# Optimization experiments

Measured on AMD Instinct MI355X. Metric: run time of the kernel, lower is better.

Reference implementation:

```python
import jax, jax.numpy as jnp
import numpy as np

N_NODES = 80000
N_EDGES = 1280000
NODE_DIM = 32
EDGE_DIM = 16
HIDDEN = 64
N_HIDDEN_LAYERS = 3  # layer_count - 1
NUM_GRAPHS = 256


def setup_inputs() -> dict:
    key = jax.random.key(0)
    ks = jax.random.split(key, 16)
    s = 0.05
    H = jax.random.normal(ks[0], (N_NODES, NODE_DIM), dtype=jnp.float32)
    Xe = jax.random.normal(ks[1], (N_EDGES, EDGE_DIM), dtype=jnp.float32)
    id_Xe = jax.random.randint(ks[2], (2, N_EDGES), 0, N_NODES, dtype=jnp.int32).astype(jnp.int64)
    batch_idx = jnp.sort(jax.random.randint(ks[3], (N_NODES,), 0, NUM_GRAPHS, dtype=jnp.int32)).astype(jnp.int64)
    # input layer: M: (node+edge)->hidden, U: (hidden+node)->hidden
    Mw0 = jax.random.normal(ks[4], (NODE_DIM + EDGE_DIM, HIDDEN), dtype=jnp.float32) * s
    Mb0 = jnp.zeros((HIDDEN,), dtype=jnp.float32)
    Uw0 = jax.random.normal(ks[5], (HIDDEN + NODE_DIM, HIDDEN), dtype=jnp.float32) * s
    Ub0 = jnp.zeros((HIDDEN,), dtype=jnp.float32)
    # hidden layers: M: (hidden+edge)->hidden, U: (2*hidden)->hidden (stacked)
    Mw_h = jax.random.normal(ks[6], (N_HIDDEN_LAYERS, HIDDEN + EDGE_DIM, HIDDEN), dtype=jnp.float32) * s
    Mb_h = jnp.zeros((N_HIDDEN_LAYERS, HIDDEN), dtype=jnp.float32)
    Uw_h = jax.random.normal(ks[7], (N_HIDDEN_LAYERS, 2 * HIDDEN, HIDDEN), dtype=jnp.float32) * s
    Ub_h = jnp.zeros((N_HIDDEN_LAYERS, HIDDEN), dtype=jnp.float32)
    # final linear head hidden -> 1
    Ww = jax.random.normal(ks[8], (HIDDEN, 1), dtype=jnp.float32) * s
    Wb = jnp.zeros((1,), dtype=jnp.float32)
    return {"H": H, "Xe": Xe, "id_Xe": id_Xe, "batch_idx": batch_idx,
            "Mw0": Mw0, "Mb0": Mb0, "Uw0": Uw0, "Ub0": Ub0,
            "Mw_h": Mw_h, "Mb_h": Mb_h, "Uw_h": Uw_h, "Ub_h": Ub_h,
            "Ww": Ww, "Wb": Wb}


def reference(H, Xe, id_Xe, batch_idx, Mw0, Mb0, Uw0, Ub0, Mw_h, Mb_h, Uw_h, Ub_h, Ww, Wb):
    n = H.shape[0]
    src = id_Xe[0]
    dst = id_Xe[1]

    def gnn_layer(h, Mw, Mb, Uw, Ub):
        # message: gather source node features, concat edge features, MLP M
        m = jax.nn.relu(jnp.concatenate([h[src], Xe], axis=-1) @ Mw + Mb)  # [E, hidden]
        # scatter-sum to target nodes
        agg = jax.ops.segment_sum(m, dst, num_segments=n)  # [N, hidden]
        # update: concat node state with aggregated message, MLP U
        return jax.nn.relu(jnp.concatenate([h, agg], axis=-1) @ Uw + Ub)

    y = gnn_layer(H, Mw0, Mb0, Uw0, Ub0)
    for i in range(Mw_h.shape[0]):
        y = gnn_layer(y, Mw_h[i], Mb_h[i], Uw_h[i], Ub_h[i])

    pooled = jax.ops.segment_sum(y, batch_idx, num_segments=NUM_GRAPHS)  # [G, hidden]
    return pooled @ Ww + Wb  # [G, 1]
```

## Files before the change

kernel.cpp:

```cpp
#include <hip/hip_runtime.h>
#include <hip/hip_fp16.h>

#define HID 64

struct alignas(8)  H4 { __half2 a, b; };
struct alignas(16) H8 { __half2 h[4]; };

typedef _Float16 h2n __attribute__((ext_vector_type(2)));

__device__ inline float dot2f(__half2 a, __half2 b, float c) {
#if __has_builtin(__builtin_amdgcn_fdot2)
    h2n an, bn;
    __builtin_memcpy(&an, &a, 4);
    __builtin_memcpy(&bn, &b, 4);
    return __builtin_amdgcn_fdot2(an, bn, c, false);
#else
    float2 af = __half22float2(a), bf = __half22float2(b);
    return c + af.x * bf.x + af.y * bf.y;
#endif
}

__global__ __launch_bounds__(256) void deg_count(const int* __restrict__ dst,
                                                 int* __restrict__ deg, int E) {
    int e = blockIdx.x * 256 + threadIdx.x;
    if (e < E) atomicAdd(&deg[dst[e]], 1);
}

__global__ __launch_bounds__(256) void scan1(const int* __restrict__ deg,
                                             int* __restrict__ rowptr,
                                             int* __restrict__ bsums, int N) {
    __shared__ int s[256];
    const int t = threadIdx.x;
    const int base = blockIdx.x * 2048 + t * 8;
    int v[8], tot = 0;
    #pragma unroll
    for (int i = 0; i < 8; i++) {
        int x = (base + i < N) ? deg[base + i] : 0;
        v[i] = tot; tot += x;
    }
    s[t] = tot; __syncthreads();
    for (int off = 1; off < 256; off <<= 1) {
        int a = (t >= off) ? s[t - off] : 0;
        __syncthreads(); s[t] += a; __syncthreads();
    }
    const int texcl = s[t] - tot;
    #pragma unroll
    for (int i = 0; i < 8; i++)
        if (base + i < N) rowptr[base + i] = texcl + v[i];
    if (t == 255) bsums[blockIdx.x] = s[255];
}

__global__ void scan2(int* bsums, int NB) {
    if (blockIdx.x == 0 && threadIdx.x == 0) {
        int run = 0;
        for (int i = 0; i < NB; i++) { int x = bsums[i]; bsums[i] = run; run += x; }
    }
}

__global__ __launch_bounds__(256) void scan3(int* __restrict__ rowptr,
                                             const int* __restrict__ bsums,
                                             int N, int E) {
    int idx = blockIdx.x * 256 + threadIdx.x;
    if (idx < N) rowptr[idx] += bsums[idx >> 11];
    if (idx == 0) rowptr[N] = E;
}

__global__ __launch_bounds__(256) void permute_k(
    const int* __restrict__ src, const int* __restrict__ dst,
    const int* __restrict__ rowptr, int* __restrict__ cursor,
    const float* __restrict__ Xe, __half* __restrict__ Xes,
    unsigned* __restrict__ pks, int E)
{
    int e = blockIdx.x * 256 + threadIdx.x;
    if (e >= E) return;
    int d = dst[e];
    int pos = rowptr[d] + atomicAdd(&cursor[d], 1);
    pks[pos] = ((unsigned)src[e] << 5) | (unsigned)(d & 31);
    const float4* xi = (const float4*)&Xe[(size_t)e * 16];
    float4 x0 = xi[0], x1 = xi[1], x2 = xi[2], x3 = xi[3];
    H8 h0, h1;
    h0.h[0] = __float22half2_rn(make_float2(x0.x, x0.y));
    h0.h[1] = __float22half2_rn(make_float2(x0.z, x0.w));
    h0.h[2] = __float22half2_rn(make_float2(x1.x, x1.y));
    h0.h[3] = __float22half2_rn(make_float2(x1.z, x1.w));
    h1.h[0] = __float22half2_rn(make_float2(x2.x, x2.y));
    h1.h[1] = __float22half2_rn(make_float2(x2.z, x2.w));
    h1.h[2] = __float22half2_rn(make_float2(x3.x, x3.y));
    h1.h[3] = __float22half2_rn(make_float2(x3.z, x3.w));
    H8* xo = (H8*)&Xes[(size_t)pos * 16];
    xo[0] = h0; xo[1] = h1;
}

template<int K1>
__global__ __launch_bounds__(256) void pm_dual(
    const float* __restrict__ Hn,
    const float* __restrict__ Wm, const float* __restrict__ bm,
    const float* __restrict__ Wu, const float* __restrict__ bu,
    __half* __restrict__ PMh, __half* __restrict__ Th, int N)
{
    constexpr int KP = K1 + 4;
    constexpr int P4 = K1 / 4;
    __shared__ float Ws[K1 * 128];
    __shared__ float Xs[32 * KP];

    const int tid = threadIdx.x;
    for (int i = tid; i < K1 * 32; i += 256) {
        const int row = i >> 5, c4 = i & 31;
        float4 v = (c4 < 16) ? *(const float4*)&Wm[row * 64 + c4 * 4]
                             : *(const float4*)&Wu[row * 64 + (c4 - 16) * 4];
        *(float4*)&Ws[row * 128 + c4 * 4] = v;
    }
    const int nbase = blockIdx.x * 32;
    for (int i = tid; i < 32 * P4; i += 256) {
        const int nl = i / P4, part = i % P4;
        const int n = nbase + nl;
        if (n < N)
            *(float4*)&Xs[nl * KP + part * 4] =
                *(const float4*)&Hn[(size_t)n * K1 + part * 4];
    }
    __syncthreads();

    const int c0 = (tid & 31) * 4;
    const int n0 = (tid >> 5) * 4;
    const float4 bv = (c0 < 64) ? *(const float4*)&bm[c0]
                                : *(const float4*)&bu[c0 - 64];

    float4 acc[4];
    #pragma unroll
    for (int i = 0; i < 4; i++) acc[i] = bv;

    #pragma unroll 4
    for (int k = 0; k < K1; k += 4) {
        const float4 w0 = *(const float4*)&Ws[(k + 0) * 128 + c0];
        const float4 w1 = *(const float4*)&Ws[(k + 1) * 128 + c0];
        const float4 w2 = *(const float4*)&Ws[(k + 2) * 128 + c0];
        const float4 w3 = *(const float4*)&Ws[(k + 3) * 128 + c0];
        #pragma unroll
        for (int ni = 0; ni < 4; ni++) {
            const float4 xv = *(const float4*)&Xs[(n0 + ni) * KP + k];
            acc[ni].x += xv.x * w0.x + xv.y * w1.x + xv.z * w2.x + xv.w * w3.x;
            acc[ni].y += xv.x * w0.y + xv.y * w1.y + xv.z * w2.y + xv.w * w3.y;
            acc[ni].z += xv.x * w0.z + xv.y * w1.z + xv.z * w2.z + xv.w * w3.z;
            acc[ni].w += xv.x * w0.w + xv.y * w1.w + xv.z * w2.w + xv.w * w3.w;
        }
    }

    #pragma unroll
    for (int ni = 0; ni < 4; ni++) {
        const int n = nbase + n0 + ni;
        if (n < N) {
            H4 o;
            o.a = __float22half2_rn(make_float2(acc[ni].x, acc[ni].y));
            o.b = __float22half2_rn(make_float2(acc[ni].z, acc[ni].w));
            if (c0 < 64) *(H4*)&PMh[(size_t)n * 64 + c0]      = o;
            else         *(H4*)&Th [(size_t)n * 64 + c0 - 64] = o;
        }
    }
}

__global__ __launch_bounds__(256) void edge_fused(
    const __half*   __restrict__ PMh,
    const __half*   __restrict__ Th,
    const __half*   __restrict__ Xes,
    const unsigned* __restrict__ pks,
    const int*      __restrict__ rowptr,
    const float*    __restrict__ Mwb,
    const float*    __restrict__ Uwb,
    float*          __restrict__ Yout,
    int N)
{
    constexpr int AGP = HID + 4;
    __shared__ float aggs[32 * AGP];

    const int tid  = threadIdx.x;
    const int wv   = tid >> 6;
    const int lane = tid & 63;
    const int c0   = (lane & 15) * 4;
    const int g    = lane >> 4;

    __half2 wh[8][4];
    #pragma unroll
    for (int p = 0; p < 8; p++)
        #pragma unroll
        for (int j = 0; j < 4; j++)
            wh[p][j] = __float22half2_rn(make_float2(Mwb[(2 * p) * 64 + c0 + j],
                                                     Mwb[(2 * p + 1) * 64 + c0 + j]));

    for (int i = tid; i < 32 * AGP; i += 256) aggs[i] = 0.f;

    const int nbase  = blockIdx.x * 32;
    const int nend   = (nbase + 32 < N) ? nbase + 32 : N;
    const int estart = rowptr[nbase];
    const int eend   = rowptr[nend];
    __syncthreads();

    int pc = estart + wv * 16;
    unsigned pk_c[4], pk_n[4], pk_n2[4];
    H4 ph_c[4], ph_n[4];
    H8 xh_c[4][2], xh_n[4][2];

    if (pc < eend) {
        #pragma unroll
        for (int s = 0; s < 4; s++) {
            const int pe = pc + g * 4 + s;
            pk_c[s] = pks[pe < eend ? pe : eend - 1];
        }
        if (pc + 64 < eend) {
            #pragma unroll
            for (int s = 0; s < 4; s++) {
                const int pe = pc + 64 + g * 4 + s;
                pk_n[s] = pks[pe < eend ? pe : eend - 1];
            }
        }
        #pragma unroll
        for (int s = 0; s < 4; s++) {
            const int pe  = pc + g * 4 + s;
            const int pcl = pe < eend ? pe : eend - 1;
            ph_c[s] = *(const H4*)&PMh[(size_t)(pk_c[s] >> 5) * 64 + c0];
            const H8* xr = (const H8*)&Xes[(size_t)pcl * 16];
            xh_c[s][0] = xr[0]; xh_c[s][1] = xr[1];
        }
    }

    for (; pc < eend; pc += 64) {
        const int pn  = pc + 64;
        const int pn2 = pc + 128;

        if (pn < eend) {
            #pragma unroll
            for (int s = 0; s < 4; s++) {
                const int pe  = pn + g * 4 + s;
                const int pcl = pe < eend ? pe : eend - 1;
                ph_n[s] = *(const H4*)&PMh[(size_t)(pk_n[s] >> 5) * 64 + c0];
                const H8* xr = (const H8*)&Xes[(size_t)pcl * 16];
                xh_n[s][0] = xr[0]; xh_n[s][1] = xr[1];
            }
        }
        if (pn2 < eend) {
            #pragma unroll
            for (int s = 0; s < 4; s++) {
                const int pe = pn2 + g * 4 + s;
                pk_n2[s] = pks[pe < eend ? pe : eend - 1];
            }
        }

        int ld_prev = -1;
        float4 racc = make_float4(0.f, 0.f, 0.f, 0.f);
        #pragma unroll
        for (int s = 0; s < 4; s++) {
            const bool valid = (pc + g * 4 + s) < eend;
            const float2 pl = __half22float2(ph_c[s].a);
            const float2 pu = __half22float2(ph_c[s].b);
            float a0 = pl.x, a1 = pl.y, a2 = pu.x, a3 = pu.y;
            #pragma unroll
            for (int p = 0; p < 8; p++) {
                const __half2 xv = xh_c[s][p >> 2].h[p & 3];
                a0 = dot2f(xv, wh[p][0], a0);
                a1 = dot2f(xv, wh[p][1], a1);
                a2 = dot2f(xv, wh[p][2], a2);
                a3 = dot2f(xv, wh[p][3], a3);
            }
            float4 v;
            v.x = fmaxf(a0, 0.f); v.y = fmaxf(a1, 0.f);
            v.z = fmaxf(a2, 0.f); v.w = fmaxf(a3, 0.f);
            const int ld = valid ? (int)(pk_c[s] & 31u) : -1;
            if (ld == ld_prev) {
                racc.x += v.x; racc.y += v.y; racc.z += v.z; racc.w += v.w;
            } else {
                if (ld_prev >= 0) {
                    float* a = &aggs[ld_prev * AGP + c0];
                    atomicAdd(a + 0, racc.x); atomicAdd(a + 1, racc.y);
                    atomicAdd(a + 2, racc.z); atomicAdd(a + 3, racc.w);
                }
                racc = v; ld_prev = ld;
            }
        }
        if (ld_prev >= 0) {
            float* a = &aggs[ld_prev * AGP + c0];
            atomicAdd(a + 0, racc.x); atomicAdd(a + 1, racc.y);
            atomicAdd(a + 2, racc.z); atomicAdd(a + 3, racc.w);
        }

        #pragma unroll
        for (int s = 0; s < 4; s++) {
            pk_c[s] = pk_n[s]; pk_n[s] = pk_n2[s];
            ph_c[s] = ph_n[s];
            xh_c[s][0] = xh_n[s][0]; xh_c[s][1] = xh_n[s][1];
        }
    }

    __syncthreads();

    {
        const int c0t = (tid & 15) * 4;
        const int r0  = tid >> 4;
        const int r1  = r0 + 16;
        const int n0g = nbase + r0, n1g = nbase + r1;
        float4 acc0 = make_float4(0.f, 0.f, 0.f, 0.f);
        float4 acc1 = make_float4(0.f, 0.f, 0.f, 0.f);
        if (n0g < N) {
            H4 th = *(const H4*)&Th[(size_t)n0g * 64 + c0t];
            float2 lo = __half22float2(th.a), hi = __half22float2(th.b);
            acc0 = make_float4(lo.x, lo.y, hi.x, hi.y);
        }
        if (n1g < N) {
            H4 th = *(const H4*)&Th[(size_t)n1g * 64 + c0t];
            float2 lo = __half22float2(th.a), hi = __half22float2(th.b);
            acc1 = make_float4(lo.x, lo.y, hi.x, hi.y);
        }
        #pragma unroll 4
        for (int k = 0; k < 64; k += 4) {
            const float4 w0 = *(const float4*)&Uwb[(k + 0) * 64 + c0t];
            const float4 w1 = *(const float4*)&Uwb[(k + 1) * 64 + c0t];
            const float4 w2 = *(const float4*)&Uwb[(k + 2) * 64 + c0t];
            const float4 w3 = *(const float4*)&Uwb[(k + 3) * 64 + c0t];
            const float4 x0 = *(const float4*)&aggs[r0 * AGP + k];
            const float4 x1 = *(const float4*)&aggs[r1 * AGP + k];
            acc0.x += x0.x * w0.x + x0.y * w1.x + x0.z * w2.x + x0.w * w3.x;
            acc0.y += x0.x * w0.y + x0.y * w1.y + x0.z * w2.y + x0.w * w3.y;
            acc0.z += x0.x * w0.z + x0.y * w1.z + x0.z * w2.z + x0.w * w3.z;
            acc0.w += x0.x * w0.w + x0.y * w1.w + x0.z * w2.w + x0.w * w3.w;
            acc1.x += x1.x * w0.x + x1.y * w1.x + x1.z * w2.x + x1.w * w3.x;
            acc1.y += x1.x * w0.y + x1.y * w1.y + x1.z * w2.y + x1.w * w3.y;
            acc1.z += x1.x * w0.z + x1.y * w1.z + x1.z * w2.z + x1.w * w3.z;
            acc1.w += x1.x * w0.w + x1.y * w1.w + x1.z * w2.w + x1.w * w3.w;
        }
        if (n0g < N) {
            float4 o;
            o.x = fmaxf(acc0.x, 0.f); o.y = fmaxf(acc0.y, 0.f);
            o.z = fmaxf(acc0.z, 0.f); o.w = fmaxf(acc0.w, 0.f);
            *(float4*)&Yout[(size_t)n0g * HID + c0t] = o;
        }
        if (n1g < N) {
            float4 o;
            o.x = fmaxf(acc1.x, 0.f); o.y = fmaxf(acc1.y, 0.f);
            o.z = fmaxf(acc1.z, 0.f); o.w = fmaxf(acc1.w, 0.f);
            *(float4*)&Yout[(size_t)n1g * HID + c0t] = o;
        }
    }
}

__global__ __launch_bounds__(256) void pool_head(
    const float* __restrict__ Y, const int* __restrict__ bidx,
    const float* __restrict__ Ww, const float* __restrict__ Wb,
    float* __restrict__ out, int N)
{
    const int g = blockIdx.x;
    int a = 0, b = N;
    while (a < b) { int m = (a + b) >> 1; if (bidx[m] < g) a = m + 1; else b = m; }
    const int lo = a;
    b = N;
    while (a < b) { int m = (a + b) >> 1; if (bidx[m] < g + 1) a = m + 1; else b = m; }
    const int hi = a;

    const int tid = threadIdx.x;
    const int c4 = tid & 15, nl = tid >> 4;
    float4 s = make_float4(0.f, 0.f, 0.f, 0.f);
    for (int n = lo + nl; n < hi; n += 16) {
        const float4 v = *(const float4*)&Y[(size_t)n * HID + c4 * 4];
        s.x += v.x; s.y += v.y; s.z += v.z; s.w += v.w;
    }
    __shared__ float red[16 * 68];
    *(float4*)&red[nl * 68 + c4 * 4] = s;
    __syncthreads();
    if (tid < 64) {
        float t = 0.f;
        #pragma unroll
        for (int r = 0; r < 16; r++) t += red[r * 68 + tid];
        t *= Ww[tid];
        #pragma unroll
        for (int off = 32; off; off >>= 1) t += __shfl_down(t, off);
        if (tid == 0) out[g] = t + Wb[0];
    }
}

extern "C" void kernel_launch(void* const* d_in, const int* in_sizes, int n_in,
                              void* d_out, int out_size, void* d_ws, size_t ws_size,
                              hipStream_t stream) {
    const float* H    = (const float*)d_in[0];
    const float* Xe   = (const float*)d_in[1];
    const int*   ids  = (const int*)d_in[2];
    const int*   bidx = (const int*)d_in[3];
    const float* Mw0  = (const float*)d_in[4];
    const float* Mb0  = (const float*)d_in[5];
    const float* Uw0  = (const float*)d_in[6];
    const float* Ub0  = (const float*)d_in[7];
    const float* MwH  = (const float*)d_in[8];
    const float* MbH  = (const float*)d_in[9];
    const float* UwH  = (const float*)d_in[10];
    const float* UbH  = (const float*)d_in[11];
    const float* Ww   = (const float*)d_in[12];
    const float* Wb   = (const float*)d_in[13];
    float* out = (float*)d_out;

    const int N = in_sizes[0] / 32;
    const int E = in_sizes[1] / 16;
    const int* src = ids;
    const int* dst = ids + E;

    float*  hbuf = (float*)d_ws;
    __half* PMh  = (__half*)(hbuf + (size_t)N * HID);
    __half* Th   = PMh + (size_t)N * HID;
    __half* Xes  = Th  + (size_t)N * HID;
    unsigned* pks = (unsigned*)(Xes + (size_t)E * 16);
    int* rowptr  = (int*)(pks + E);
    int* deg     = rowptr + (N + 1);
    int* bsums   = deg + N;

    const int NB = (N + 2047) / 2048;
    const int eblocks = (E + 255) / 256;
    const int ntile   = (N + 31) / 32;

    hipMemsetAsync(deg, 0, (size_t)N * sizeof(int), stream);
    deg_count<<<eblocks, 256, 0, stream>>>(dst, deg, E);
    scan1<<<NB, 256, 0, stream>>>(deg, rowptr, bsums, N);
    scan2<<<1, 64, 0, stream>>>(bsums, NB);
    scan3<<<(N + 255) / 256, 256, 0, stream>>>(rowptr, bsums, N, E);
    hipMemsetAsync(deg, 0, (size_t)N * sizeof(int), stream);
    permute_k<<<eblocks, 256, 0, stream>>>(src, dst, rowptr, deg,
                                           Xe, Xes, pks, E);

    pm_dual<32><<<ntile, 256, 0, stream>>>(H, Mw0, Mb0, Uw0, Ub0, PMh, Th, N);
    edge_fused<<<ntile, 256, 0, stream>>>(PMh, Th, Xes, pks, rowptr,
                                          Mw0 + 32 * HID, Uw0 + 32 * HID, hbuf, N);

    for (int l = 0; l < 3; l++) {
        const float* Mw = MwH + (size_t)l * 80 * HID;
        const float* Uw = UwH + (size_t)l * 128 * HID;
        pm_dual<64><<<ntile, 256, 0, stream>>>(hbuf, Mw, MbH + (size_t)l * HID,
                                               Uw, UbH + (size_t)l * HID, PMh, Th, N);
        edge_fused<<<ntile, 256, 0, stream>>>(PMh, Th, Xes, pks, rowptr,
                                              Mw + 64 * HID, Uw + 64 * HID, hbuf, N);
    }

    pool_head<<<256, 256, 0, stream>>>(hbuf, bidx, Ww, Wb, out, N);
}
```

Measured before the change: 967.2 us.

## Restructure edge kernel with 64-node tiles and LDS-staged triple-buffered edge features

The edge aggregation kernel now handles 64 destination nodes per block, which widens the packed local-destination field to 6 bits. Edge features are loaded coalesced as 8-byte chunks into a per-wave LDS buffer. A three-stage register and LDS pipeline overlaps the index, gather and feature loads several iterations ahead of compute. The intent is better memory-level parallelism and fewer blocks, at the cost of more LDS per block and reads clamped against the global edge count. Weight loads also become vectorized float4 reads.

```diff
diff --git a/kernel.cpp b/kernel.cpp
--- a/kernel.cpp
+++ b/kernel.cpp
@@ -75,7 +75,7 @@
     if (e >= E) return;
     int d = dst[e];
     int pos = rowptr[d] + atomicAdd(&cursor[d], 1);
-    pks[pos] = ((unsigned)src[e] << 5) | (unsigned)(d & 31);
+    pks[pos] = ((unsigned)src[e] << 6) | (unsigned)(d & 63);
     const float4* xi = (const float4*)&Xe[(size_t)e * 16];
     float4 x0 = xi[0], x1 = xi[1], x2 = xi[2], x3 = xi[3];
     H8 h0, h1;
@@ -167,146 +167,161 @@
     const float*    __restrict__ Mwb,
     const float*    __restrict__ Uwb,
     float*          __restrict__ Yout,
-    int N)
+    int N, int Etot)
 {
-    constexpr int AGP = HID + 4;
-    __shared__ float aggs[32 * AGP];
+    constexpr int TILE = 64;
+    constexpr int AGP  = HID + 4;
+    __shared__ float  aggs[TILE * AGP];
+    __shared__ __half xsh[4][3][512];
 
     const int tid  = threadIdx.x;
     const int wv   = tid >> 6;
     const int lane = tid & 63;
     const int c0   = (lane & 15) * 4;
     const int g    = lane >> 4;
+    const int Ecap = Etot - 16;
 
     __half2 wh[8][4];
     #pragma unroll
-    for (int p = 0; p < 8; p++)
-        #pragma unroll
-        for (int j = 0; j < 4; j++)
-            wh[p][j] = __float22half2_rn(make_float2(Mwb[(2 * p) * 64 + c0 + j],
-                                                     Mwb[(2 * p + 1) * 64 + c0 + j]));
-
-    for (int i = tid; i < 32 * AGP; i += 256) aggs[i] = 0.f;
-
-    const int nbase  = blockIdx.x * 32;
-    const int nend   = (nbase + 32 < N) ? nbase + 32 : N;
+    for (int p = 0; p < 8; p++) {
+        const float4 r0 = *(const float4*)&Mwb[(2 * p) * 64 + c0];
+        const float4 r1 = *(const float4*)&Mwb[(2 * p + 1) * 64 + c0];
+        wh[p][0] = __float22half2_rn(make_float2(r0.x, r1.x));
+        wh[p][1] = __float22half2_rn(make_float2(r0.y, r1.y));
+        wh[p][2] = __float22half2_rn(make_float2(r0.z, r1.z));
+        wh[p][3] = __float22half2_rn(make_float2(r0.w, r1.w));
+    }
+
+    for (int i = tid; i < TILE * AGP; i += 256) aggs[i] = 0.f;
+
+    const int nbase  = blockIdx.x * TILE;
+    const int nend   = (nbase + TILE < N) ? nbase + TILE : N;
     const int estart = rowptr[nbase];
     const int eend   = rowptr[nend];
+
+    unsigned pk_r[3][4];
+    unsigned ldp[3];
+    H4       ph[3][4];
+    uint2    xt[3];
+
+    const int exc   = lane >> 2;
+    const int xpart = lane & 3;
+    const int woff  = exc * 32 + ((exc & 4) << 1) + xpart * 4;
+
+#define ISSUE_X(ST2, PC) do {                                                 \
+    const int pbX_ = ((PC) <= Ecap) ? (PC) : Ecap;                            \
+    xt[ST2] = *(const uint2*)&Xes[((size_t)(pbX_ + exc)) * 16 + xpart * 4];   \
+} while (0)
+
+#define ISSUE_PK(ST2, PC) do {                                                \
+    const int pbK_ = ((PC) <= Ecap) ? (PC) : Ecap;                            \
+    _Pragma("unroll")                                                         \
+    for (int s = 0; s < 4; s++) pk_r[ST2][s] = pks[pbK_ + g * 4 + s];         \
+} while (0)
+
+#define ISSUE_G(ST2) do {                                                     \
+    unsigned l_ = 0;                                                          \
+    _Pragma("unroll")                                                         \
+    for (int s = 0; s < 4; s++) {                                             \
+        const unsigned pk_ = pk_r[ST2][s];                                    \
+        ph[ST2][s] = *(const H4*)&PMh[(size_t)(pk_ >> 6) * 64 + c0];          \
+        l_ |= (pk_ & 63u) << (s * 8);                                         \
+    }                                                                         \
+    ldp[ST2] = l_;                                                            \
+} while (0)
+
+#define WRITE_X(ST2)                                                          \
+    *(uint2*)&xsh[wv][ST2][woff] = xt[ST2]
+
+#define COMPUTE(ST, PC) do {                                                  \
+    int ld_prev = -1;                                                         \
+    float4 racc = make_float4(0.f, 0.f, 0.f, 0.f);                            \
+    _Pragma("unroll")                                                         \
+    for (int s = 0; s < 4; s++) {                                             \
+        const int e_  = g * 4 + s;                                            \
+        const int eo_ = e_ * 32 + ((e_ & 4) << 1);                            \
+        const H8 x0 = *(const H8*)&xsh[wv][ST][eo_];                          \
+        const H8 x1 = *(const H8*)&xsh[wv][ST][eo_ + 8];                      \
+        const float2 pl = __half22float2(ph[ST][s].a);                        \
+        const float2 pu = __half22float2(ph[ST][s].b);                        \
+        float a0 = pl.x, a1 = pl.y, a2 = pu.x, a3 = pu.y;                     \
+        _Pragma("unroll")                                                     \
+        for (int p = 0; p < 4; p++) {                                         \
+            const __half2 xv = x0.h[p];                                       \
+            a0 = dot2f(xv, wh[p][0], a0); a1 = dot2f(xv, wh[p][1], a1);       \
+            a2 = dot2f(xv, wh[p][2], a2); a3 = dot2f(xv, wh[p][3], a3);       \
+        }                                                                     \
+        _Pragma("unroll")                                                     \
+        for (int p = 0; p < 4; p++) {                                         \
+            const __half2 xv = x1.h[p];                                       \
+            a0 = dot2f(xv, wh[p+4][0], a0); a1 = dot2f(xv, wh[p+4][1], a1);   \
+            a2 = dot2f(xv, wh[p+4][2], a2); a3 = dot2f(xv, wh[p+4][3], a3);   \
+        }                                                                     \
+        float4 v;                                                             \
+        v.x = fmaxf(a0, 0.f); v.y = fmaxf(a1, 0.f);                           \
+        v.z = fmaxf(a2, 0.f); v.w = fmaxf(a3, 0.f);                           \
+        const int ld = ((PC) + e_ < eend)                                     \
+                     ? (int)((ldp[ST] >> (s * 8)) & 63u) : -1;                \
+        if (ld == ld_prev) {                                                  \
+            racc.x += v.x; racc.y += v.y; racc.z += v.z; racc.w += v.w;       \
+        } else {                                                              \
+            if (ld_prev >= 0) {                                               \
+                float* a_ = &aggs[ld_prev * AGP + c0];                        \
+                atomicAdd(a_ + 0, racc.x); atomicAdd(a_ + 1, racc.y);         \
+                atomicAdd(a_ + 2, racc.z); atomicAdd(a_ + 3, racc.w);         \
+            }                                                                 \
+            racc = v; ld_prev = ld;                                           \
+        }                                                                     \
+    }                                                                         \
+    if (ld_prev >= 0) {                                                       \
+        float* a_ = &aggs[ld_prev * AGP + c0];                                \
+        atomicAdd(a_ + 0, racc.x); atomicAdd(a_ + 1, racc.y);                 \
+        atomicAdd(a_ + 2, racc.z); atomicAdd(a_ + 3, racc.w);                 \
+    }                                                                         \
+} while (0)
+
+    const int pc0 = estart + wv * 16;
+
+    ISSUE_X(0, pc0); ISSUE_X(1, pc0 + 64); ISSUE_X(2, pc0 + 128);
+    ISSUE_PK(0, pc0); ISSUE_PK(1, pc0 + 64); ISSUE_PK(2, pc0 + 128);
+    ISSUE_G(0); WRITE_X(0);
+    ISSUE_G(1); WRITE_X(1);
+    ISSUE_PK(0, pc0 + 192);
+    ISSUE_X(0, pc0 + 192);
+
     __syncthreads();
 
-    int pc = estart + wv * 16;
-    unsigned pk_c[4], pk_n[4], pk_n2[4];
-    H4 ph_c[4], ph_n[4];
-    H8 xh_c[4][2], xh_n[4][2];
-
-    if (pc < eend) {
-        #pragma unroll
-        for (int s = 0; s < 4; s++) {
-            const int pe = pc + g * 4 + s;
-            pk_c[s] = pks[pe < eend ? pe : eend - 1];
-        }
-        if (pc + 64 < eend) {
-            #pragma unroll
-            for (int s = 0; s < 4; s++) {
-                const int pe = pc + 64 + g * 4 + s;
-                pk_n[s] = pks[pe < eend ? pe : eend - 1];
-            }
-        }
-        #pragma unroll
-        for (int s = 0; s < 4; s++) {
-            const int pe  = pc + g * 4 + s;
-            const int pcl = pe < eend ? pe : eend - 1;
-            ph_c[s] = *(const H4*)&PMh[(size_t)(pk_c[s] >> 5) * 64 + c0];
-            const H8* xr = (const H8*)&Xes[(size_t)pcl * 16];
-            xh_c[s][0] = xr[0]; xh_c[s][1] = xr[1];
-        }
-    }
-
-    for (; pc < eend; pc += 64) {
-        const int pn  = pc + 64;
-        const int pn2 = pc + 128;
-
-        if (pn < eend) {
-            #pragma unroll
-            for (int s = 0; s < 4; s++) {
-                const int pe  = pn + g * 4 + s;
-                const int pcl = pe < eend ? pe : eend - 1;
-                ph_n[s] = *(const H4*)&PMh[(size_t)(pk_n[s] >> 5) * 64 + c0];
-                const H8* xr = (const H8*)&Xes[(size_t)pcl * 16];
-                xh_n[s][0] = xr[0]; xh_n[s][1] = xr[1];
-            }
-        }
-        if (pn2 < eend) {
-            #pragma unroll
-            for (int s = 0; s < 4; s++) {
-                const int pe = pn2 + g * 4 + s;
-                pk_n2[s] = pks[pe < eend ? pe : eend - 1];
-            }
-        }
-
-        int ld_prev = -1;
-        float4 racc = make_float4(0.f, 0.f, 0.f, 0.f);
-        #pragma unroll
-        for (int s = 0; s < 4; s++) {
-            const bool valid = (pc + g * 4 + s) < eend;
-            const float2 pl = __half22float2(ph_c[s].a);
-            const float2 pu = __half22float2(ph_c[s].b);
-            float a0 = pl.x, a1 = pl.y, a2 = pu.x, a3 = pu.y;
-            #pragma unroll
-            for (int p = 0; p < 8; p++) {
-                const __half2 xv = xh_c[s][p >> 2].h[p & 3];
-                a0 = dot2f(xv, wh[p][0], a0);
-                a1 = dot2f(xv, wh[p][1], a1);
-                a2 = dot2f(xv, wh[p][2], a2);
-                a3 = dot2f(xv, wh[p][3], a3);
-            }
-            float4 v;
-            v.x = fmaxf(a0, 0.f); v.y = fmaxf(a1, 0.f);
-            v.z = fmaxf(a2, 0.f); v.w = fmaxf(a3, 0.f);
-            const int ld = valid ? (int)(pk_c[s] & 31u) : -1;
-            if (ld == ld_prev) {
-                racc.x += v.x; racc.y += v.y; racc.z += v.z; racc.w += v.w;
-            } else {
-                if (ld_prev >= 0) {
-                    float* a = &aggs[ld_prev * AGP + c0];
-                    atomicAdd(a + 0, racc.x); atomicAdd(a + 1, racc.y);
-                    atomicAdd(a + 2, racc.z); atomicAdd(a + 3, racc.w);
-                }
-                racc = v; ld_prev = ld;
-            }
-        }
-        if (ld_prev >= 0) {
-            float* a = &aggs[ld_prev * AGP + c0];
-            atomicAdd(a + 0, racc.x); atomicAdd(a + 1, racc.y);
-            atomicAdd(a + 2, racc.z); atomicAdd(a + 3, racc.w);
-        }
-
-        #pragma unroll
-        for (int s = 0; s < 4; s++) {
-            pk_c[s] = pk_n[s]; pk_n[s] = pk_n2[s];
-            ph_c[s] = ph_n[s];
-            xh_c[s][0] = xh_n[s][0]; xh_c[s][1] = xh_n[s][1];
-        }
-    }
+    for (int pc = pc0; pc < eend; ) {
+        { ISSUE_X(1, pc + 256); ISSUE_PK(1, pc + 256); ISSUE_G(2); WRITE_X(2); COMPUTE(0, pc); }
+        pc += 64; if (pc >= eend) break;
+        { ISSUE_X(2, pc + 256); ISSUE_PK(2, pc + 256); ISSUE_G(0); WRITE_X(0); COMPUTE(1, pc); }
+        pc += 64; if (pc >= eend) break;
+        { ISSUE_X(0, pc + 256); ISSUE_PK(0, pc + 256); ISSUE_G(1); WRITE_X(1); COMPUTE(2, pc); }
+        pc += 64;
+    }
+
+#undef ISSUE_X
+#undef ISSUE_PK
+#undef ISSUE_G
+#undef WRITE_X
+#undef COMPUTE
 
     __syncthreads();
 
     {
         const int c0t = (tid & 15) * 4;
         const int r0  = tid >> 4;
-        const int r1  = r0 + 16;
-        const int n0g = nbase + r0, n1g = nbase + r1;
-        float4 acc0 = make_float4(0.f, 0.f, 0.f, 0.f);
-        float4 acc1 = make_float4(0.f, 0.f, 0.f, 0.f);
-        if (n0g < N) {
-            H4 th = *(const H4*)&Th[(size_t)n0g * 64 + c0t];
-            float2 lo = __half22float2(th.a), hi = __half22float2(th.b);
-            acc0 = make_float4(lo.x, lo.y, hi.x, hi.y);
-        }
-        if (n1g < N) {
-            H4 th = *(const H4*)&Th[(size_t)n1g * 64 + c0t];
-            float2 lo = __half22float2(th.a), hi = __half22float2(th.b);
-            acc1 = make_float4(lo.x, lo.y, hi.x, hi.y);
+        float4 acc[4];
+        #pragma unroll
+        for (int j = 0; j < 4; j++) {
+            const int n = nbase + r0 + 16 * j;
+            if (n < N) {
+                H4 th = *(const H4*)&Th[(size_t)n * 64 + c0t];
+                float2 lo = __half22float2(th.a), hi = __half22float2(th.b);
+                acc[j] = make_float4(lo.x, lo.y, hi.x, hi.y);
+            } else {
+                acc[j] = make_float4(0.f, 0.f, 0.f, 0.f);
+            }
         }
         #pragma unroll 4
         for (int k = 0; k < 64; k += 4) {
@@ -314,28 +329,24 @@
             const float4 w1 = *(const float4*)&Uwb[(k + 1) * 64 + c0t];
             const float4 w2 = *(const float4*)&Uwb[(k + 2) * 64 + c0t];
             const float4 w3 = *(const float4*)&Uwb[(k + 3) * 64 + c0t];
-            const float4 x0 = *(const float4*)&aggs[r0 * AGP + k];
-            const float4 x1 = *(const float4*)&aggs[r1 * AGP + k];
-            acc0.x += x0.x * w0.x + x0.y * w1.x + x0.z * w2.x + x0.w * w3.x;
-            acc0.y += x0.x * w0.y + x0.y * w1.y + x0.z * w2.y + x0.w * w3.y;
-            acc0.z += x0.x * w0.z + x0.y * w1.z + x0.z * w2.z + x0.w * w3.z;
-            acc0.w += x0.x * w0.w + x0.y * w1.w + x0.z * w2.w + x0.w * w3.w;
-            acc1.x += x1.x * w0.x + x1.y * w1.x + x1.z * w2.x + x1.w * w3.x;
-            acc1.y += x1.x * w0.y + x1.y * w1.y + x1.z * w2.y + x1.w * w3.y;
-            acc1.z += x1.x * w0.z + x1.y * w1.z + x1.z * w2.z + x1.w * w3.z;
-            acc1.w += x1.x * w0.w + x1.y * w1.w + x1.z * w2.w + x1.w * w3.w;
+            #pragma unroll
+            for (int j = 0; j < 4; j++) {
+                const float4 x = *(const float4*)&aggs[(r0 + 16 * j) * AGP + k];
+                acc[j].x += x.x * w0.x + x.y * w1.x + x.z * w2.x + x.w * w3.x;
+                acc[j].y += x.x * w0.y + x.y * w1.y + x.z * w2.y + x.w * w3.y;
+                acc[j].z += x.x * w0.z + x.y * w1.z + x.z * w2.z + x.w * w3.z;
+                acc[j].w += x.x * w0.w + x.y * w1.w + x.z * w2.w + x.w * w3.w;
+            }
         }
-        if (n0g < N) {
-            float4 o;
-            o.x = fmaxf(acc0.x, 0.f); o.y = fmaxf(acc0.y, 0.f);
-            o.z = fmaxf(acc0.z, 0.f); o.w = fmaxf(acc0.w, 0.f);
-            *(float4*)&Yout[(size_t)n0g * HID + c0t] = o;
-        }
-        if (n1g < N) {
-            float4 o;
-            o.x = fmaxf(acc1.x, 0.f); o.y = fmaxf(acc1.y, 0.f);
-            o.z = fmaxf(acc1.z, 0.f); o.w = fmaxf(acc1.w, 0.f);
-            *(float4*)&Yout[(size_t)n1g * HID + c0t] = o;
+        #pragma unroll
+        for (int j = 0; j < 4; j++) {
+            const int n = nbase + r0 + 16 * j;
+            if (n < N) {
+                float4 o;
+                o.x = fmaxf(acc[j].x, 0.f); o.y = fmaxf(acc[j].y, 0.f);
+                o.z = fmaxf(acc[j].z, 0.f); o.w = fmaxf(acc[j].w, 0.f);
+                *(float4*)&Yout[(size_t)n * HID + c0t] = o;
+            }
         }
     }
 }
@@ -409,7 +420,8 @@
 
     const int NB = (N + 2047) / 2048;
     const int eblocks = (E + 255) / 256;
-    const int ntile   = (N + 31) / 32;
+    const int ntile32 = (N + 31) / 32;
+    const int ntile64 = (N + 63) / 64;
 
     hipMemsetAsync(deg, 0, (size_t)N * sizeof(int), stream);
     deg_count<<<eblocks, 256, 0, stream>>>(dst, deg, E);
@@ -420,17 +432,17 @@
     permute_k<<<eblocks, 256, 0, stream>>>(src, dst, rowptr, deg,
                                            Xe, Xes, pks, E);
 
-    pm_dual<32><<<ntile, 256, 0, stream>>>(H, Mw0, Mb0, Uw0, Ub0, PMh, Th, N);
-    edge_fused<<<ntile, 256, 0, stream>>>(PMh, Th, Xes, pks, rowptr,
-                                          Mw0 + 32 * HID, Uw0 + 32 * HID, hbuf, N);
+    pm_dual<32><<<ntile32, 256, 0, stream>>>(H, Mw0, Mb0, Uw0, Ub0, PMh, Th, N);
+    edge_fused<<<ntile64, 256, 0, stream>>>(PMh, Th, Xes, pks, rowptr,
+                                            Mw0 + 32 * HID, Uw0 + 32 * HID, hbuf, N, E);
 
     for (int l = 0; l < 3; l++) {
         const float* Mw = MwH + (size_t)l * 80 * HID;
         const float* Uw = UwH + (size_t)l * 128 * HID;
-        pm_dual<64><<<ntile, 256, 0, stream>>>(hbuf, Mw, MbH + (size_t)l * HID,
-                                               Uw, UbH + (size_t)l * HID, PMh, Th, N);
-        edge_fused<<<ntile, 256, 0, stream>>>(PMh, Th, Xes, pks, rowptr,
-                                              Mw + 64 * HID, Uw + 64 * HID, hbuf, N);
+        pm_dual<64><<<ntile32, 256, 0, stream>>>(hbuf, Mw, MbH + (size_t)l * HID,
+                                                 Uw, UbH + (size_t)l * HID, PMh, Th, N);
+        edge_fused<<<ntile64, 256, 0, stream>>>(PMh, Th, Xes, pks, rowptr,
+                                                Mw + 64 * HID, Uw + 64 * HID, hbuf, N, E);
     }
 
     pool_head<<<256, 256, 0, stream>>>(hbuf, bidx, Ww, Wb, out, N);
```

Result: slower. 1.014 ms (+4.9%).

## Use MFMA for edge-feature message matmul with swizzled PM layout and deeper prefetch

Applied to the files above, without the earlier changes.

Replaces the per-lane fdot2 loop in the edge kernel with 16x16x32 f16 MFMA instructions. The edge features (K=16, zero-padded to 32 via a lane mask) form the A operand and the weight slice forms B. The PM buffer is stored in a column-interleaved layout so each lane's gathered 8 bytes line up with the MFMA accumulator layout. Packed keys and Xe rows are loaded cooperatively and broadcast with shuffles, under a 4-stage software-pipelined rotation. The aim is to cut VALU cost in the edge kernel, at the price of a scattered 2-byte store pattern in pm_dual and more register pressure.

```diff
diff --git a/kernel.cpp b/kernel.cpp
--- a/kernel.cpp
+++ b/kernel.cpp
@@ -6,19 +6,8 @@
 struct alignas(8)  H4 { __half2 a, b; };
 struct alignas(16) H8 { __half2 h[4]; };
 
-typedef _Float16 h2n __attribute__((ext_vector_type(2)));
-
-__device__ inline float dot2f(__half2 a, __half2 b, float c) {
-#if __has_builtin(__builtin_amdgcn_fdot2)
-    h2n an, bn;
-    __builtin_memcpy(&an, &a, 4);
-    __builtin_memcpy(&bn, &b, 4);
-    return __builtin_amdgcn_fdot2(an, bn, c, false);
-#else
-    float2 af = __half22float2(a), bf = __half22float2(b);
-    return c + af.x * bf.x + af.y * bf.y;
-#endif
-}
+typedef _Float16 f16x8 __attribute__((ext_vector_type(8)));
+typedef float    f32x4 __attribute__((ext_vector_type(4)));
 
 __global__ __launch_bounds__(256) void deg_count(const int* __restrict__ dst,
                                                  int* __restrict__ deg, int E) {
@@ -75,7 +64,7 @@
     if (e >= E) return;
     int d = dst[e];
     int pos = rowptr[d] + atomicAdd(&cursor[d], 1);
-    pks[pos] = ((unsigned)src[e] << 5) | (unsigned)(d & 31);
+    pks[pos] = ((unsigned)src[e] << 6) | (unsigned)(d & 63);
     const float4* xi = (const float4*)&Xe[(size_t)e * 16];
     float4 x0 = xi[0], x1 = xi[1], x2 = xi[2], x3 = xi[3];
     H8 h0, h1;
@@ -96,7 +85,7 @@
     const float* __restrict__ Hn,
     const float* __restrict__ Wm, const float* __restrict__ bm,
     const float* __restrict__ Wu, const float* __restrict__ bu,
-    __half* __restrict__ PMh, __half* __restrict__ Th, int N)
+    __half* __restrict__ PMs, __half* __restrict__ Th, int N)
 {
     constexpr int KP = K1 + 4;
     constexpr int P4 = K1 / 4;
@@ -149,17 +138,24 @@
     for (int ni = 0; ni < 4; ni++) {
         const int n = nbase + n0 + ni;
         if (n < N) {
-            H4 o;
-            o.a = __float22half2_rn(make_float2(acc[ni].x, acc[ni].y));
-            o.b = __float22half2_rn(make_float2(acc[ni].z, acc[ni].w));
-            if (c0 < 64) *(H4*)&PMh[(size_t)n * 64 + c0]      = o;
-            else         *(H4*)&Th [(size_t)n * 64 + c0 - 64] = o;
+            if (c0 < 64) {
+                const int cb = c0 & 15, hb = c0 >> 4;
+                PMs[(size_t)n * 64 + (cb + 0) * 4 + hb] = __float2half_rn(acc[ni].x);
+                PMs[(size_t)n * 64 + (cb + 1) * 4 + hb] = __float2half_rn(acc[ni].y);
+                PMs[(size_t)n * 64 + (cb + 2) * 4 + hb] = __float2half_rn(acc[ni].z);
+                PMs[(size_t)n * 64 + (cb + 3) * 4 + hb] = __float2half_rn(acc[ni].w);
+            } else {
+                H4 o;
+                o.a = __float22half2_rn(make_float2(acc[ni].x, acc[ni].y));
+                o.b = __float22half2_rn(make_float2(acc[ni].z, acc[ni].w));
+                *(H4*)&Th[(size_t)n * 64 + c0 - 64] = o;
+            }
         }
     }
 }
 
 __global__ __launch_bounds__(256) void edge_fused(
-    const __half*   __restrict__ PMh,
+    const __half*   __restrict__ PMs,
     const __half*   __restrict__ Th,
     const __half*   __restrict__ Xes,
     const unsigned* __restrict__ pks,
@@ -167,7 +163,7 @@
     const float*    __restrict__ Mwb,
     const float*    __restrict__ Uwb,
     float*          __restrict__ Yout,
-    int N)
+    int N, int Etot)
 {
     constexpr int AGP = HID + 4;
     __shared__ float aggs[32 * AGP];
@@ -175,16 +171,20 @@
     const int tid  = threadIdx.x;
     const int wv   = tid >> 6;
     const int lane = tid & 63;
-    const int c0   = (lane & 15) * 4;
-    const int g    = lane >> 4;
-
-    __half2 wh[8][4];
+    const int q    = lane >> 4;
+    const int li   = lane & 15;
+    const int sl0  = q * 4;
+
+    f16x8 bfr[4];
     #pragma unroll
-    for (int p = 0; p < 8; p++)
+    for (int b = 0; b < 4; b++) {
         #pragma unroll
-        for (int j = 0; j < 4; j++)
-            wh[p][j] = __float22half2_rn(make_float2(Mwb[(2 * p) * 64 + c0 + j],
-                                                     Mwb[(2 * p + 1) * 64 + c0 + j]));
+        for (int i = 0; i < 8; i++) {
+            float w = (q < 2) ? Mwb[(8 * q + i) * 64 + 16 * b + li] : 0.f;
+            bfr[b][i] = (_Float16)w;
+        }
+    }
+    const unsigned amask = (q < 2) ? 0xFFFFFFFFu : 0u;
 
     for (int i = tid; i < 32 * AGP; i += 256) aggs[i] = 0.f;
 
@@ -194,100 +194,115 @@
     const int eend   = rowptr[nend];
     __syncthreads();
 
-    int pc = estart + wv * 16;
-    unsigned pk_c[4], pk_n[4], pk_n2[4];
-    H4 ph_c[4], ph_n[4];
-    H8 xh_c[4][2], xh_n[4][2];
-
-    if (pc < eend) {
-        #pragma unroll
-        for (int s = 0; s < 4; s++) {
-            const int pe = pc + g * 4 + s;
-            pk_c[s] = pks[pe < eend ? pe : eend - 1];
-        }
-        if (pc + 64 < eend) {
-            #pragma unroll
-            for (int s = 0; s < 4; s++) {
-                const int pe = pc + 64 + g * 4 + s;
-                pk_n[s] = pks[pe < eend ? pe : eend - 1];
-            }
-        }
-        #pragma unroll
-        for (int s = 0; s < 4; s++) {
-            const int pe  = pc + g * 4 + s;
-            const int pcl = pe < eend ? pe : eend - 1;
-            ph_c[s] = *(const H4*)&PMh[(size_t)(pk_c[s] >> 5) * 64 + c0];
-            const H8* xr = (const H8*)&Xes[(size_t)pcl * 16];
-            xh_c[s][0] = xr[0]; xh_c[s][1] = xr[1];
-        }
-    }
-
-    for (; pc < eend; pc += 64) {
-        const int pn  = pc + 64;
-        const int pn2 = pc + 128;
-
-        if (pn < eend) {
-            #pragma unroll
-            for (int s = 0; s < 4; s++) {
-                const int pe  = pn + g * 4 + s;
-                const int pcl = pe < eend ? pe : eend - 1;
-                ph_n[s] = *(const H4*)&PMh[(size_t)(pk_n[s] >> 5) * 64 + c0];
-                const H8* xr = (const H8*)&Xes[(size_t)pcl * 16];
-                xh_n[s][0] = xr[0]; xh_n[s][1] = xr[1];
-            }
-        }
-        if (pn2 < eend) {
-            #pragma unroll
-            for (int s = 0; s < 4; s++) {
-                const int pe = pn2 + g * 4 + s;
-                pk_n2[s] = pks[pe < eend ? pe : eend - 1];
-            }
-        }
-
-        int ld_prev = -1;
-        float4 racc = make_float4(0.f, 0.f, 0.f, 0.f);
-        #pragma unroll
-        for (int s = 0; s < 4; s++) {
-            const bool valid = (pc + g * 4 + s) < eend;
-            const float2 pl = __half22float2(ph_c[s].a);
-            const float2 pu = __half22float2(ph_c[s].b);
-            float a0 = pl.x, a1 = pl.y, a2 = pu.x, a3 = pu.y;
-            #pragma unroll
-            for (int p = 0; p < 8; p++) {
-                const __half2 xv = xh_c[s][p >> 2].h[p & 3];
-                a0 = dot2f(xv, wh[p][0], a0);
-                a1 = dot2f(xv, wh[p][1], a1);
-                a2 = dot2f(xv, wh[p][2], a2);
-                a3 = dot2f(xv, wh[p][3], a3);
-            }
-            float4 v;
-            v.x = fmaxf(a0, 0.f); v.y = fmaxf(a1, 0.f);
-            v.z = fmaxf(a2, 0.f); v.w = fmaxf(a3, 0.f);
-            const int ld = valid ? (int)(pk_c[s] & 31u) : -1;
-            if (ld == ld_prev) {
-                racc.x += v.x; racc.y += v.y; racc.z += v.z; racc.w += v.w;
-            } else {
-                if (ld_prev >= 0) {
-                    float* a = &aggs[ld_prev * AGP + c0];
-                    atomicAdd(a + 0, racc.x); atomicAdd(a + 1, racc.y);
-                    atomicAdd(a + 2, racc.z); atomicAdd(a + 3, racc.w);
-                }
-                racc = v; ld_prev = ld;
-            }
-        }
-        if (ld_prev >= 0) {
-            float* a = &aggs[ld_prev * AGP + c0];
-            atomicAdd(a + 0, racc.x); atomicAdd(a + 1, racc.y);
-            atomicAdd(a + 2, racc.z); atomicAdd(a + 3, racc.w);
-        }
-
-        #pragma unroll
-        for (int s = 0; s < 4; s++) {
-            pk_c[s] = pk_n[s]; pk_n[s] = pk_n2[s];
-            ph_c[s] = ph_n[s];
-            xh_c[s][0] = xh_n[s][0]; xh_c[s][1] = xh_n[s][1];
-        }
-    }
+    const int pc0 = estart + wv * 16;
+    const int qXl = q * 64 + li;
+
+    unsigned pkv[2];
+    uint4    xq[4];
+    H4       ph[4][4];
+    unsigned ldp[4];
+
+#define LOAD_PKV(B, CB) do {                                                  \
+    int e_ = (CB) + qXl; e_ = e_ < Etot - 1 ? e_ : Etot - 1;                  \
+    pkv[B] = pks[e_];                                                         \
+} while (0)
+
+#define LOAD_XQ(S, CB) do {                                                   \
+    int b_ = (CB); b_ = b_ <= Etot - 16 ? b_ : Etot - 16;                     \
+    xq[S] = *(const uint4*)((const char*)Xes + (size_t)(b_ + li) * 32         \
+                            + ((q & 1) << 4));                                \
+} while (0)
+
+#define GATH(S, PB, D4) do {                                                  \
+    unsigned l_ = 0;                                                          \
+    _Pragma("unroll")                                                         \
+    for (int j = 0; j < 4; j++) {                                             \
+        unsigned pk_ = (unsigned)__shfl((int)pkv[PB], (D4) * 16 + sl0 + j);   \
+        ph[S][j] = *(const H4*)((const char*)PMs +                            \
+                                ((size_t)(pk_ >> 6) << 7) + li * 8);          \
+        l_ |= (pk_ & 31u) << (8 * j);                                         \
+    }                                                                         \
+    ldp[S] = l_;                                                              \
+} while (0)
+
+#define COMPUTE(S, PCC) do {                                                  \
+    uint4 xa = xq[S];                                                         \
+    xa.x &= amask; xa.y &= amask; xa.z &= amask; xa.w &= amask;               \
+    f16x8 a; __builtin_memcpy(&a, &xa, 16);                                   \
+    f32x4 acc0, acc1, acc2, acc3;                                             \
+    _Pragma("unroll")                                                         \
+    for (int j = 0; j < 4; j++) {                                             \
+        const float2 g0 = __half22float2(ph[S][j].a);                         \
+        const float2 g1 = __half22float2(ph[S][j].b);                         \
+        acc0[j] = g0.x; acc1[j] = g0.y; acc2[j] = g1.x; acc3[j] = g1.y;       \
+    }                                                                         \
+    acc0 = __builtin_amdgcn_mfma_f32_16x16x32_f16(a, bfr[0], acc0, 0, 0, 0);  \
+    acc1 = __builtin_amdgcn_mfma_f32_16x16x32_f16(a, bfr[1], acc1, 0, 0, 0);  \
+    acc2 = __builtin_amdgcn_mfma_f32_16x16x32_f16(a, bfr[2], acc2, 0, 0, 0);  \
+    acc3 = __builtin_amdgcn_mfma_f32_16x16x32_f16(a, bfr[3], acc3, 0, 0, 0);  \
+    int ld_prev = -1;                                                         \
+    f32x4 racc = {0.f, 0.f, 0.f, 0.f};                                        \
+    _Pragma("unroll")                                                         \
+    for (int j = 0; j < 4; j++) {                                             \
+        f32x4 v;                                                              \
+        v[0] = fmaxf(acc0[j], 0.f); v[1] = fmaxf(acc1[j], 0.f);               \
+        v[2] = fmaxf(acc2[j], 0.f); v[3] = fmaxf(acc3[j], 0.f);               \
+        const int ld = ((PCC) + sl0 + j < eend)                               \
+                     ? (int)((ldp[S] >> (8 * j)) & 31u) : -1;                 \
+        if (ld == ld_prev) {                                                  \
+            racc[0] += v[0]; racc[1] += v[1];                                 \
+            racc[2] += v[2]; racc[3] += v[3];                                 \
+        } else {                                                              \
+            if (ld_prev >= 0) {                                               \
+                float* a_ = &aggs[ld_prev * AGP + li];                        \
+                atomicAdd(a_ +  0, racc[0]); atomicAdd(a_ + 16, racc[1]);     \
+                atomicAdd(a_ + 32, racc[2]); atomicAdd(a_ + 48, racc[3]);     \
+            }                                                                 \
+            racc = v; ld_prev = ld;                                           \
+        }                                                                     \
+    }                                                                         \
+    if (ld_prev >= 0) {                                                       \
+        float* a_ = &aggs[ld_prev * AGP + li];                                \
+        atomicAdd(a_ +  0, racc[0]); atomicAdd(a_ + 16, racc[1]);             \
+        atomicAdd(a_ + 32, racc[2]); atomicAdd(a_ + 48, racc[3]);             \
+    }                                                                         \
+} while (0)
+
+    if (pc0 < eend) {
+        LOAD_PKV(0, pc0);
+        LOAD_PKV(1, pc0 + 256);
+        LOAD_XQ(0, pc0);       LOAD_XQ(1, pc0 + 64);
+        LOAD_XQ(2, pc0 + 128); LOAD_XQ(3, pc0 + 192);
+        GATH(0, 0, 0);
+        GATH(1, 0, 1);
+
+        int pc = pc0;
+        while (true) {
+            { GATH(2, 0, 2); COMPUTE(0, pc); LOAD_XQ(0, pc + 256); }
+            pc += 64; if (pc >= eend) break;
+            { GATH(3, 0, 3); COMPUTE(1, pc); LOAD_XQ(1, pc + 256); }
+            pc += 64; if (pc >= eend) break;
+            { GATH(0, 1, 0); COMPUTE(2, pc); LOAD_XQ(2, pc + 256);
+              LOAD_PKV(0, pc + 384); }
+            pc += 64; if (pc >= eend) break;
+            { GATH(1, 1, 1); COMPUTE(3, pc); LOAD_XQ(3, pc + 256); }
+            pc += 64; if (pc >= eend) break;
+            { GATH(2, 1, 2); COMPUTE(0, pc); LOAD_XQ(0, pc + 256); }
+            pc += 64; if (pc >= eend) break;
+            { GATH(3, 1, 3); COMPUTE(1, pc); LOAD_XQ(1, pc + 256); }
+            pc += 64; if (pc >= eend) break;
+            { GATH(0, 0, 0); COMPUTE(2, pc); LOAD_XQ(2, pc + 256);
+              LOAD_PKV(1, pc + 384); }
+            pc += 64; if (pc >= eend) break;
+            { GATH(1, 0, 1); COMPUTE(3, pc); LOAD_XQ(3, pc + 256); }
+            pc += 64; if (pc >= eend) break;
+        }
+    }
+
+#undef LOAD_PKV
+#undef LOAD_XQ
+#undef GATH
+#undef COMPUTE
 
     __syncthreads();
 
@@ -399,8 +414,8 @@
     const int* dst = ids + E;
 
     float*  hbuf = (float*)d_ws;
-    __half* PMh  = (__half*)(hbuf + (size_t)N * HID);
-    __half* Th   = PMh + (size_t)N * HID;
+    __half* PMs  = (__half*)(hbuf + (size_t)N * HID);
+    __half* Th   = PMs + (size_t)N * HID;
     __half* Xes  = Th  + (size_t)N * HID;
     unsigned* pks = (unsigned*)(Xes + (size_t)E * 16);
     int* rowptr  = (int*)(pks + E);
@@ -409,7 +424,7 @@
 
     const int NB = (N + 2047) / 2048;
     const int eblocks = (E + 255) / 256;
-    const int ntile   = (N + 31) / 32;
+    const int ntile32 = (N + 31) / 32;
 
     hipMemsetAsync(deg, 0, (size_t)N * sizeof(int), stream);
     deg_count<<<eblocks, 256, 0, stream>>>(dst, deg, E);
@@ -420,17 +435,17 @@
     permute_k<<<eblocks, 256, 0, stream>>>(src, dst, rowptr, deg,
                                            Xe, Xes, pks, E);
 
-    pm_dual<32><<<ntile, 256, 0, stream>>>(H, Mw0, Mb0, Uw0, Ub0, PMh, Th, N);
-    edge_fused<<<ntile, 256, 0, stream>>>(PMh, Th, Xes, pks, rowptr,
-                                          Mw0 + 32 * HID, Uw0 + 32 * HID, hbuf, N);
+    pm_dual<32><<<ntile32, 256, 0, stream>>>(H, Mw0, Mb0, Uw0, Ub0, PMs, Th, N);
+    edge_fused<<<ntile32, 256, 0, stream>>>(PMs, Th, Xes, pks, rowptr,
+                                            Mw0 + 32 * HID, Uw0 + 32 * HID, hbuf, N, E);
 
     for (int l = 0; l < 3; l++) {
         const float* Mw = MwH + (size_t)l * 80 * HID;
         const float* Uw = UwH + (size_t)l * 128 * HID;
-        pm_dual<64><<<ntile, 256, 0, stream>>>(hbuf, Mw, MbH + (size_t)l * HID,
-                                               Uw, UbH + (size_t)l * HID, PMh, Th, N);
-        edge_fused<<<ntile, 256, 0, stream>>>(PMh, Th, Xes, pks, rowptr,
-                                              Mw + 64 * HID, Uw + 64 * HID, hbuf, N);
+        pm_dual<64><<<ntile32, 256, 0, stream>>>(hbuf, Mw, MbH + (size_t)l * HID,
+                                                 Uw, UbH + (size_t)l * HID, PMs, Th, N);
+        edge_fused<<<ntile32, 256, 0, stream>>>(PMs, Th, Xes, pks, rowptr,
+                                                Mw + 64 * HID, Uw + 64 * HID, hbuf, N, E);
     }
 
     pool_head<<<256, 256, 0, stream>>>(hbuf, bidx, Ww, Wb, out, N);
```

Measured after the change: 995.0 us. 2.9% more time.
